# Performance work log

Measured on AMD Instinct MI355X. Metric: run time of the kernel, lower is better.

Reference implementation:

```python
import jax, jax.numpy as jnp
import numpy as np

NUM_ELECTRODES = 19
NUM_WINDOWS = 30
NUM_FREQS = 128
HEADS = 8
HID = 80
BATCH = 16
D_OUT = HEADS * HID  # 640


def _build_edge_index(num_nodes, num_windows):
    # spatiotemporal graph: dense intra-window blocks (incl. self-loops)
    # + bidirectional temporal edges between same electrode in adjacent windows
    srcs, dsts = [], []
    for w in range(num_windows):
        idx = np.arange(num_nodes) + w * num_nodes
        s, d = np.meshgrid(idx, idx, indexing='ij')
        srcs.append(s.ravel()); dsts.append(d.ravel())
    for w in range(num_windows - 1):
        a = np.arange(num_nodes) + w * num_nodes
        b = a + num_nodes
        srcs.append(a); dsts.append(b)
        srcs.append(b); dsts.append(a)
    return np.stack([np.concatenate(srcs), np.concatenate(dsts)]).astype(np.int32)


def setup_inputs() -> dict:
    key = jax.random.key(0)
    ks = jax.random.split(key, 12)
    f = NUM_FREQS
    x = jax.random.normal(ks[0], (BATCH, NUM_WINDOWS, NUM_FREQS, NUM_ELECTRODES), jnp.float32)
    s_in = 1.0 / np.sqrt(f)
    s_h = 1.0 / np.sqrt(D_OUT)
    Wl = jax.random.normal(ks[1], (D_OUT, f), jnp.float32) * s_in
    bl = jax.random.normal(ks[2], (D_OUT,), jnp.float32) * s_in
    Wr = jax.random.normal(ks[3], (D_OUT, f), jnp.float32) * s_in
    br = jax.random.normal(ks[4], (D_OUT,), jnp.float32) * s_in
    att = jax.random.normal(ks[5], (HEADS, HID), jnp.float32) * (1.0 / np.sqrt(HID))
    conv_bias = jax.random.normal(ks[6], (D_OUT,), jnp.float32) * 0.01
    Wpool = jax.random.normal(ks[7], (1, D_OUT), jnp.float32) * s_h
    bpool = jax.random.normal(ks[8], (1,), jnp.float32) * s_h
    Wfc = jax.random.normal(ks[9], (1, D_OUT), jnp.float32) * s_h
    bfc = jax.random.normal(ks[10], (1,), jnp.float32) * s_h
    edge_index = jnp.asarray(_build_edge_index(NUM_ELECTRODES, NUM_WINDOWS))
    return {"x": x, "edge_index": edge_index, "Wl": Wl, "bl": bl, "Wr": Wr, "br": br,
            "att": att, "conv_bias": conv_bias, "Wpool": Wpool, "bpool": bpool,
            "Wfc": Wfc, "bfc": bfc}


def reference(x, edge_index, Wl, bl, Wr, br, att, conv_bias, Wpool, bpool, Wfc, bfc):
    B, W, F, E19 = x.shape
    N = W * E19
    H, C = att.shape
    # (B, W, F, E) -> (B, W, E, F) -> (B, N, F)
    nodes = x.transpose(0, 1, 3, 2).reshape(B, N, F)
    src, dst = edge_index[0], edge_index[1]
    # GATv2: lin_l on source (messages), lin_r on target
    xl = (nodes @ Wl.T + bl).reshape(B, N, H, C)
    xr = (nodes @ Wr.T + br).reshape(B, N, H, C)
    msg = xl[:, src]                        # (B, E, H, C) source features
    key_feat = msg + xr[:, dst]             # (B, E, H, C)
    e = jnp.einsum('behc,hc->beh', jax.nn.leaky_relu(key_feat, 0.2), att)  # (B,E,H)

    def seg_softmax(e_b):  # (E, H), segment softmax over dst
        m = jax.ops.segment_max(e_b, dst, num_segments=N)
        ex = jnp.exp(e_b - m[dst])
        s = jax.ops.segment_sum(ex, dst, num_segments=N)
        return ex / (s[dst] + 1e-16)

    alpha = jax.vmap(seg_softmax)(e)        # (B, E, H)
    agg = jax.vmap(lambda m: jax.ops.segment_sum(m, dst, num_segments=N))(
        msg * alpha[..., None])             # (B, N, H, C)
    out = agg.reshape(B, N, H * C) + conv_bias
    out = jax.nn.elu(out)
    scores = out @ Wpool.T + bpool          # (B, N, 1)
    attn = jax.nn.softmax(scores, axis=1)
    pooled = (attn * out).sum(axis=1)       # (B, H*C)
    logits = pooled @ Wfc.T + bfc           # (B, 1)
    return logits.squeeze(1)
```

## Files before the change

### kernel.cpp

```cpp
#include <hip/hip_runtime.h>
#include <math.h>

#define B   16
#define NW  30
#define NE  19
#define NF  128
#define NH  8
#define NC  80
#define ND  640
#define NN  570
#define NROW (B*NN)

typedef _Float16 f16x2 __attribute__((ext_vector_type(2)));
typedef _Float16 f16x4 __attribute__((ext_vector_type(4)));
typedef _Float16 f16x8 __attribute__((ext_vector_type(8)));
typedef float    f32x16 __attribute__((ext_vector_type(16)));

#define WT_OFF   0
#define WT_SZ    (1280*128)
#define XL_OFF   (WT_OFF + WT_SZ)
#define XLR16_SZ (B*NN*ND/2)
#define XR_OFF   (XL_OFF + XLR16_SZ)
#define XT_OFF   (XR_OFF + XLR16_SZ)
#define SCP_OFF  (XT_OFF + 2*(NROW*NF/2))
#define SCP_SZ   (NH*B*NN)
#define QP_OFF   (SCP_OFF + SCP_SZ)

__global__ __launch_bounds__(256) void k0_prep(const float* __restrict__ Wl,
                                               const float* __restrict__ Wr,
                                               const float* __restrict__ x,
                                               _Float16* __restrict__ wph,
                                               _Float16* __restrict__ wpl,
                                               _Float16* __restrict__ xph,
                                               _Float16* __restrict__ xpl){
  int bx = blockIdx.x, t = threadIdx.x;
  if (bx < 160){
    int i = bx*256 + t;
    int dd = i >> 5, k = (i & 31) * 4;
    const float* srcp = (dd < 640) ? (Wl + dd*NF + k) : (Wr + (dd-640)*NF + k);
    float4 v = *(const float4*)srcp;
    _Float16 h0=(_Float16)v.x, h1=(_Float16)v.y, h2=(_Float16)v.z, h3=(_Float16)v.w;
    f16x4 hv = {h0, h1, h2, h3};
    f16x4 lv = {(_Float16)(v.x-(float)h0), (_Float16)(v.y-(float)h1),
                (_Float16)(v.z-(float)h2), (_Float16)(v.w-(float)h3)};
    int s = k >> 4, hh = (k >> 3) & 1, off = k & 7;
    size_t chunk = (((size_t)(dd >> 5)*8 + s)*64 + hh*32 + (dd & 31))*8 + off;
    *(f16x4*)(wph + chunk) = hv;
    *(f16x4*)(wpl + chunk) = lv;
    return;
  }
  int wb = bx - 160, w = wb % NW, b = wb / NW;
  __shared__ float ns[19*132];
  const float4* xs = (const float4*)(x + (size_t)((b*NW + w)*NF)*NE);
  for (int i = t; i < 608; i += 256){
    float4 v = xs[i];
    int idx = 4*i;
    float vv[4] = {v.x, v.y, v.z, v.w};
    #pragma unroll
    for (int k = 0; k < 4; ++k){
      int f = (idx + k) / NE, el = (idx + k) % NE;
      ns[el*132 + f] = vv[k];
    }
  }
  __syncthreads();
  for (int i = t; i < 608; i += 256){
    int el = i >> 5, k = (i & 31) * 4;
    float4 v = *(const float4*)&ns[el*132 + k];
    _Float16 h0=(_Float16)v.x, h1=(_Float16)v.y, h2=(_Float16)v.z, h3=(_Float16)v.w;
    f16x4 hv = {h0, h1, h2, h3};
    f16x4 lv = {(_Float16)(v.x-(float)h0), (_Float16)(v.y-(float)h1),
                (_Float16)(v.z-(float)h2), (_Float16)(v.w-(float)h3)};
    int n = (b*NW + w)*NE + el;
    int s = k >> 4, hh = (k >> 3) & 1, off = k & 7;
    size_t chunk = (((size_t)(n >> 5)*8 + s)*64 + hh*32 + (n & 31))*8 + off;
    *(f16x4*)(xph + chunk) = hv;
    *(f16x4*)(xpl + chunk) = lv;
  }
}

__global__ __launch_bounds__(256) void k1_gemm(const _Float16* __restrict__ xph,
                                               const _Float16* __restrict__ xpl,
                                               const _Float16* __restrict__ wph,
                                               const _Float16* __restrict__ wpl,
                                               const float* __restrict__ bl,
                                               const float* __restrict__ br,
                                               _Float16* __restrict__ xl,
                                               _Float16* __restrict__ xr){
  int wave = threadIdx.x >> 6, lane = threadIdx.x & 63;
  int mt = blockIdx.x;
  int nt = blockIdx.y*4 + wave;

  const f16x8* pah = (const f16x8*)xph + (size_t)mt*8*64 + lane;
  const f16x8* pal = (const f16x8*)xpl + (size_t)mt*8*64 + lane;
  const f16x8* pbh = (const f16x8*)wph + (size_t)nt*8*64 + lane;
  const f16x8* pbl = (const f16x8*)wpl + (size_t)nt*8*64 + lane;

  f32x16 acc = {};
  #pragma unroll
  for (int s = 0; s < 8; ++s){
    f16x8 a_h = pah[s*64];
    f16x8 b_h = pbh[s*64];
    f16x8 a_l = pal[s*64];
    f16x8 b_l = pbl[s*64];
    acc = __builtin_amdgcn_mfma_f32_32x32x16_f16(a_h, b_h, acc, 0, 0, 0);
    acc = __builtin_amdgcn_mfma_f32_32x32x16_f16(a_l, b_h, acc, 0, 0, 0);
    acc = __builtin_amdgcn_mfma_f32_32x32x16_f16(a_h, b_l, acc, 0, 0, 0);
  }

  int bn = nt*32 + (lane & 31);
  float bias = (bn < 640) ? bl[bn] : br[bn - 640];
  _Float16* dstb = (bn < 640) ? xl : xr;
  int col = (bn < 640) ? bn : bn - 640;
  int rbase = mt*32 + 4*(lane >> 5);
  #pragma unroll
  for (int r = 0; r < 16; ++r){
    int node = rbase + (r & 3) + 8*(r >> 2);
    dstb[(size_t)node*ND + col] = (_Float16)(acc[r] + bias);
  }
}

__global__ __launch_bounds__(256) void k2_gat(const _Float16* __restrict__ xl,
                                              const _Float16* __restrict__ xr,
                                              const float* __restrict__ att,
                                              const float* __restrict__ cb,
                                              const float* __restrict__ wpool,
                                              const float* __restrict__ wfc,
                                              float* __restrict__ scp,
                                              float* __restrict__ qp){
  int w = blockIdx.x, b = blockIdx.y, h = blockIdx.z, t = threadIdx.x;
  __shared__ _Float16 xl_s[57*88];
  __shared__ _Float16 xr_s[19*88];
  __shared__ _Float16 atth_s[80];
  __shared__ float cb_s[80], wp_s[80], wf_s[80];
  __shared__ float e_s[19*22];
  __shared__ float score_s[19], q_s[19];
  if (t < 19){ score_s[t] = 0.f; q_s[t] = 0.f; }
  const bool vp = (w > 0), vn = (w < NW-1);

  for (int i = t; i < 570; i += 256){
    int row = i / 10, c8 = i % 10;
    int node = -1;
    if (row < 19)        node = w*NE + row;
    else if (row < 38) { if (vp) node = (w-1)*NE + (row-19); }
    else               { if (vn) node = (w+1)*NE + (row-38); }
    if (node >= 0)
      *(f16x8*)&xl_s[row*88 + 8*c8] =
        *(const f16x8*)(xl + (size_t)(b*NN + node)*ND + h*80 + 8*c8);
  }
  for (int i = t; i < 190; i += 256){
    int row = i / 10, c8 = i % 10;
    int node = w*NE + row;
    *(f16x8*)&xr_s[row*88 + 8*c8] =
      *(const f16x8*)(xr + (size_t)(b*NN + node)*ND + h*80 + 8*c8);
  }
  if (t < 80){
    int a = t / 20, c4 = t % 20;
    if (a == 0){
      float4 v = *(const float4*)(att + h*80 + 4*c4);
      f16x4 hv = {(_Float16)v.x, (_Float16)v.y, (_Float16)v.z, (_Float16)v.w};
      *(f16x4*)&atth_s[4*c4] = hv;
    } else {
      const float* sp0 = (a == 1) ? cb + h*80 : (a == 2) ? wpool + h*80 : wfc + h*80;
      float*       dp  = (a == 1) ? cb_s      : (a == 2) ? wp_s        : wf_s;
      *(float4*)&dp[4*c4] = *(const float4*)(sp0 + 4*c4);
    }
  }
  __syncthreads();

  for (int eid = t; eid < 399; eid += 256){
    int s = eid / 19, dst = eid % 19;
    if ((s == 19 && !vp) || (s == 20 && !vn)) continue;
    int row = (s < 19) ? s : (s == 19 ? 19 + dst : 38 + dst);
    const f16x8* xlp = (const f16x8*)&xl_s[row*88];
    const f16x8* xrp = (const f16x8*)&xr_s[dst*88];
    const f16x8* ap  = (const f16x8*)atth_s;
    float acc = 0.f;
    #pragma unroll 2
    for (int c8 = 0; c8 < 10; ++c8){
      f16x8 z  = xlp[c8] + xrp[c8];
      f16x8 zs = z * (_Float16)0.2f;
      f16x8 zm = __builtin_elementwise_max(z, zs);
      f16x8 a8 = ap[c8];
#if __has_builtin(__builtin_amdgcn_fdot2)
      acc = __builtin_amdgcn_fdot2(__builtin_shufflevector(zm, zm, 0, 1),
                                   __builtin_shufflevector(a8, a8, 0, 1), acc, false);
      acc = __builtin_amdgcn_fdot2(__builtin_shufflevector(zm, zm, 2, 3),
                                   __builtin_shufflevector(a8, a8, 2, 3), acc, false);
      acc = __builtin_amdgcn_fdot2(__builtin_shufflevector(zm, zm, 4, 5),
                                   __builtin_shufflevector(a8, a8, 4, 5), acc, false);
      acc = __builtin_amdgcn_fdot2(__builtin_shufflevector(zm, zm, 6, 7),
                                   __builtin_shufflevector(a8, a8, 6, 7), acc, false);
#else
      #pragma unroll
      for (int j = 0; j < 8; ++j)
        acc = fmaf((float)zm[j], (float)a8[j], acc);
#endif
    }
    e_s[dst*22 + s] = acc;
  }
  __syncthreads();

  if (t < 19){
    float* base = &e_s[t*22];
    float m = -1e30f;
    for (int s = 0; s < 21; ++s){
      if ((s == 19 && !vp) || (s == 20 && !vn)) continue;
      m = fmaxf(m, base[s]);
    }
    float sum = 0.f;
    for (int s = 0; s < 21; ++s){
      if ((s == 19 && !vp) || (s == 20 && !vn)) continue;
      float ex = __expf(base[s] - m); base[s] = ex; sum += ex;
    }
    base[21] = 1.f / (sum + 1e-16f);
  }
  __syncthreads();

  if (t < 190){
    int dst = t / 10, c0 = (t % 10) * 8;
    float acc[8];
    #pragma unroll
    for (int j = 0; j < 8; ++j) acc[j] = 0.f;
    for (int s = 0; s < 21; ++s){
      if ((s == 19 && !vp) || (s == 20 && !vn)) continue;
      int row = (s < 19) ? s : (s == 19 ? 19 + dst : 38 + dst);
      float al = e_s[dst*22 + s];
      f16x8 v = *(const f16x8*)&xl_s[row*88 + c0];
      #pragma unroll
      for (int j = 0; j < 8; ++j) acc[j] = fmaf(al, (float)v[j], acc[j]);
    }
    float inv = e_s[dst*22 + 21];
    float sp = 0.f, fq = 0.f;
    #pragma unroll
    for (int k = 0; k < 8; ++k){
      float v = fmaf(inv, acc[k], cb_s[c0 + k]);
      v = (v > 0.f) ? v : (__expf(v) - 1.f);
      sp += v * wp_s[c0 + k];
      fq += v * wf_s[c0 + k];
    }
    atomicAdd(&score_s[dst], sp);
    atomicAdd(&q_s[dst], fq);
  }
  __syncthreads();
  if (t < 19){
    size_t o = ((size_t)h*B + b)*NN + w*NE + t;
    scp[o] = score_s[t];
    qp[o]  = q_s[t];
  }
}

__global__ __launch_bounds__(256) void k3_final(const float* __restrict__ scp,
                                                const float* __restrict__ qp,
                                                const float* __restrict__ bpool,
                                                const float* __restrict__ bfc,
                                                float* __restrict__ out){
  int b = blockIdx.x, t = threadIdx.x;
  __shared__ float ss[NN], qq[NN];
  __shared__ float red[4], rs[4], rq[4];
  float bp = bpool[0];
  for (int i = t; i < NN; i += 256){
    float v = bp, q = 0.f;
    #pragma unroll
    for (int h = 0; h < NH; ++h){
      v += scp[((size_t)h*B + b)*NN + i];
      q += qp [((size_t)h*B + b)*NN + i];
    }
    ss[i] = v; qq[i] = q;
  }
  __syncthreads();
  float m = -1e30f;
  for (int i = t; i < NN; i += 256) m = fmaxf(m, ss[i]);
  for (int off = 32; off > 0; off >>= 1) m = fmaxf(m, __shfl_down(m, off));
  int wid = t >> 6, lane = t & 63;
  if (lane == 0) red[wid] = m;
  __syncthreads();
  if (t == 0) red[0] = fmaxf(fmaxf(red[0], red[1]), fmaxf(red[2], red[3]));
  __syncthreads();
  m = red[0];
  float s = 0.f, qs = 0.f;
  for (int i = t; i < NN; i += 256){
    float e = __expf(ss[i] - m);
    s += e; qs += e * qq[i];
  }
  for (int off = 32; off > 0; off >>= 1){
    s  += __shfl_down(s, off);
    qs += __shfl_down(qs, off);
  }
  if (lane == 0){ rs[wid] = s; rq[wid] = qs; }
  __syncthreads();
  if (t == 0){
    float S = rs[0] + rs[1] + rs[2] + rs[3];
    float Q = rq[0] + rq[1] + rq[2] + rq[3];
    out[b] = Q / (S + 1e-16f) + bfc[0];
  }
}

extern "C" void kernel_launch(void* const* d_in, const int* in_sizes, int n_in,
                              void* d_out, int out_size, void* d_ws, size_t ws_size,
                              hipStream_t stream){
  const float* x     = (const float*)d_in[0];
  const float* Wl    = (const float*)d_in[2];
  const float* bl    = (const float*)d_in[3];
  const float* Wr    = (const float*)d_in[4];
  const float* br    = (const float*)d_in[5];
  const float* att   = (const float*)d_in[6];
  const float* cb    = (const float*)d_in[7];
  const float* wpool = (const float*)d_in[8];
  const float* bpool = (const float*)d_in[9];
  const float* wfc   = (const float*)d_in[10];
  const float* bfc   = (const float*)d_in[11];

  float* ws      = (float*)d_ws;
  _Float16* wph  = (_Float16*)(ws + WT_OFF);
  _Float16* wpl  = wph + 1280*NF;
  _Float16* xlb  = (_Float16*)(ws + XL_OFF);
  _Float16* xrb  = (_Float16*)(ws + XR_OFF);
  _Float16* xph  = (_Float16*)(ws + XT_OFF);
  _Float16* xpl  = xph + (size_t)NROW*NF;
  float* scp     = ws + SCP_OFF;
  float* qp      = ws + QP_OFF;

  k0_prep  <<<640, 256, 0, stream>>>(Wl, Wr, x, wph, wpl, xph, xpl);
  k1_gemm  <<<dim3(285, 10), 256, 0, stream>>>(xph, xpl, wph, wpl, bl, br, xlb, xrb);
  k2_gat   <<<dim3(NW, B, NH), 256, 0, stream>>>(xlb, xrb, att, cb, wpool, wfc, scp, qp);
  k3_final <<<B, 256, 0, stream>>>(scp, qp, bpool, bfc, (float*)d_out);
}
```

Before: 136.9 us.

## Process three windows per GAT block to reuse neighbor-window xl loads

```diff
diff --git a/kernel.cpp b/kernel.cpp
--- a/kernel.cpp
+++ b/kernel.cpp
@@ -127,29 +127,28 @@
                                               const float* __restrict__ wfc,
                                               float* __restrict__ scp,
                                               float* __restrict__ qp){
-  int w = blockIdx.x, b = blockIdx.y, h = blockIdx.z, t = threadIdx.x;
-  __shared__ _Float16 xl_s[57*88];
-  __shared__ _Float16 xr_s[19*88];
+  int wg = blockIdx.x, b = blockIdx.y, h = blockIdx.z, t = threadIdx.x;
+  const int w0 = wg*3;
+  __shared__ _Float16 xl_s[95*88];
+  __shared__ _Float16 xr_s[57*88];
   __shared__ _Float16 atth_s[80];
   __shared__ float cb_s[80], wp_s[80], wf_s[80];
-  __shared__ float e_s[19*22];
-  __shared__ float score_s[19], q_s[19];
-  if (t < 19){ score_s[t] = 0.f; q_s[t] = 0.f; }
-  const bool vp = (w > 0), vn = (w < NW-1);
-
+  __shared__ float e_s[57*22];
+  __shared__ float score_s[57], q_s[57];
+  if (t < 57){ score_s[t] = 0.f; q_s[t] = 0.f; }
+
+  for (int i = t; i < 950; i += 256){
+    int row = i / 10, c8 = i % 10;
+    int win = w0 - 1 + row/19;
+    if (win >= 0 && win < NW){
+      int node = win*NE + row%19;
+      *(f16x8*)&xl_s[row*88 + 8*c8] =
+        *(const f16x8*)(xl + (size_t)(b*NN + node)*ND + h*80 + 8*c8);
+    }
+  }
   for (int i = t; i < 570; i += 256){
     int row = i / 10, c8 = i % 10;
-    int node = -1;
-    if (row < 19)        node = w*NE + row;
-    else if (row < 38) { if (vp) node = (w-1)*NE + (row-19); }
-    else               { if (vn) node = (w+1)*NE + (row-38); }
-    if (node >= 0)
-      *(f16x8*)&xl_s[row*88 + 8*c8] =
-        *(const f16x8*)(xl + (size_t)(b*NN + node)*ND + h*80 + 8*c8);
-  }
-  for (int i = t; i < 190; i += 256){
-    int row = i / 10, c8 = i % 10;
-    int node = w*NE + row;
+    int node = (w0 + row/19)*NE + row%19;
     *(f16x8*)&xr_s[row*88 + 8*c8] =
       *(const f16x8*)(xr + (size_t)(b*NN + node)*ND + h*80 + 8*c8);
   }
@@ -167,12 +166,15 @@
   }
   __syncthreads();
 
-  for (int eid = t; eid < 399; eid += 256){
-    int s = eid / 19, dst = eid % 19;
-    if ((s == 19 && !vp) || (s == 20 && !vn)) continue;
-    int row = (s < 19) ? s : (s == 19 ? 19 + dst : 38 + dst);
+  for (int eid = t; eid < 1197; eid += 256){
+    int s = eid / 57, d = eid % 57;
+    int wl = d / 19, el = d % 19;
+    int row;
+    if (s < 19)       row = (wl+1)*19 + s;
+    else if (s == 19){ if (w0 + wl == 0)    continue; row = wl*19 + el; }
+    else              { if (w0 + wl == NW-1) continue; row = (wl+2)*19 + el; }
     const f16x8* xlp = (const f16x8*)&xl_s[row*88];
-    const f16x8* xrp = (const f16x8*)&xr_s[dst*88];
+    const f16x8* xrp = (const f16x8*)&xr_s[d*88];
     const f16x8* ap  = (const f16x8*)atth_s;
     float acc = 0.f;
     #pragma unroll 2
@@ -196,11 +198,13 @@
         acc = fmaf((float)zm[j], (float)a8[j], acc);
 #endif
     }
-    e_s[dst*22 + s] = acc;
-  }
-  __syncthreads();
-
-  if (t < 19){
+    e_s[d*22 + s] = acc;
+  }
+  __syncthreads();
+
+  if (t < 57){
+    int wl = t / 19;
+    const bool vp = (w0 + wl > 0), vn = (w0 + wl < NW-1);
     float* base = &e_s[t*22];
     float m = -1e30f;
     for (int s = 0; s < 21; ++s){
@@ -216,20 +220,24 @@
   }
   __syncthreads();
 
-  if (t < 190){
-    int dst = t / 10, c0 = (t % 10) * 8;
+  for (int slot = t; slot < 570; slot += 256){
+    int d = slot / 10, c0 = (slot % 10) * 8;
+    int wl = d / 19, el = d % 19;
+    const bool vp = (w0 + wl > 0), vn = (w0 + wl < NW-1);
     float acc[8];
     #pragma unroll
     for (int j = 0; j < 8; ++j) acc[j] = 0.f;
     for (int s = 0; s < 21; ++s){
-      if ((s == 19 && !vp) || (s == 20 && !vn)) continue;
-      int row = (s < 19) ? s : (s == 19 ? 19 + dst : 38 + dst);
-      float al = e_s[dst*22 + s];
+      int row;
+      if (s < 19)       row = (wl+1)*19 + s;
+      else if (s == 19){ if (!vp) continue; row = wl*19 + el; }
+      else              { if (!vn) continue; row = (wl+2)*19 + el; }
+      float al = e_s[d*22 + s];
       f16x8 v = *(const f16x8*)&xl_s[row*88 + c0];
       #pragma unroll
       for (int j = 0; j < 8; ++j) acc[j] = fmaf(al, (float)v[j], acc[j]);
     }
-    float inv = e_s[dst*22 + 21];
+    float inv = e_s[d*22 + 21];
     float sp = 0.f, fq = 0.f;
     #pragma unroll
     for (int k = 0; k < 8; ++k){
@@ -238,12 +246,12 @@
       sp += v * wp_s[c0 + k];
       fq += v * wf_s[c0 + k];
     }
-    atomicAdd(&score_s[dst], sp);
-    atomicAdd(&q_s[dst], fq);
-  }
-  __syncthreads();
-  if (t < 19){
-    size_t o = ((size_t)h*B + b)*NN + w*NE + t;
+    atomicAdd(&score_s[d], sp);
+    atomicAdd(&q_s[d], fq);
+  }
+  __syncthreads();
+  if (t < 57){
+    size_t o = ((size_t)h*B + b)*NN + w0*NE + t;
     scp[o] = score_s[t];
     qp[o]  = q_s[t];
   }
@@ -322,6 +330,6 @@
 
   k0_prep  <<<640, 256, 0, stream>>>(Wl, Wr, x, wph, wpl, xph, xpl);
   k1_gemm  <<<dim3(285, 10), 256, 0, stream>>>(xph, xpl, wph, wpl, bl, br, xlb, xrb);
-  k2_gat   <<<dim3(NW, B, NH), 256, 0, stream>>>(xlb, xrb, att, cb, wpool, wfc, scp, qp);
+  k2_gat   <<<dim3(10, B, NH), 256, 0, stream>>>(xlb, xrb, att, cb, wpool, wfc, scp, qp);
   k3_final <<<B, 256, 0, stream>>>(scp, qp, bpool, bfc, (float*)d_out);
 }
```

New measurement: 139.3 us. About the same (+1.7%).
